# Kernel tuning notes

Hardware: AMD Instinct MI355X
Metric: run time of the kernel (lower is better)

Reference implementation:

```python
import jax, jax.numpy as jnp
import numpy as np

SCALING = 2.0      # lora_alpha / r = 32 / 16
TEMPERATURE = 1.0  # router_temperature


def setup_inputs() -> dict:
    key = jax.random.key(0)
    ks = jax.random.split(key, 7)
    B, S, D, K, R = 4, 2048, 4096, 8, 16
    # Note: torch inits lora_B to zeros; we use small random values so the
    return {
        "x": jax.random.normal(ks[0], (B, S, D), dtype=jnp.float32),
        "base_w": jax.random.normal(ks[1], (D, D), dtype=jnp.float32) * 0.02,
        "base_b": jax.random.normal(ks[2], (D,), dtype=jnp.float32) * 0.02,
        "lora_A": jax.random.normal(ks[3], (K, R, D), dtype=jnp.float32) * 0.02,
        "lora_B": jax.random.normal(ks[4], (K, D, R), dtype=jnp.float32) * 0.02,
        "router_w": jax.random.normal(ks[5], (K, D), dtype=jnp.float32) * 0.02,
        "router_b": jnp.zeros((K,), dtype=jnp.float32),
    }


def reference(x, base_w, base_b, lora_A, lora_B, router_w, router_b):
    # base_layer(x): x @ W^T + b
    base = jnp.einsum("bsd,od->bso", x, base_w) + base_b
    # router on mean-pooled sequence (x.dim()==3 branch): softmax(Linear(mean_s x))
    router_in = x.mean(axis=1)                                   # [B, D]
    logits = router_in @ router_w.T + router_b                   # [B, K]
    weights = jax.nn.softmax(logits / TEMPERATURE, axis=-1)      # [B, K]
    # grouped LoRA experts: h = A_k x, out = sum_k w_k * B_k h  (dropout p=0 -> identity)
    h = jnp.einsum("bsd,krd->bskr", x, lora_A)                   # [B, S, K, R]
    lora = jnp.einsum("bskr,kor,bk->bso", h, lora_B, weights)    # [B, S, D]
    return base + SCALING * lora
```

## Files before the change

kernel.cpp:

```cpp
#include <hip/hip_runtime.h>
#include <hip/hip_fp16.h>
#include <stdint.h>

typedef _Float16 f16;
typedef __attribute__((ext_vector_type(8))) _Float16 f16x8;
typedef __attribute__((ext_vector_type(4))) float f32x4;

#define D_DIM 4096
#define S_DIM 2048
#define M_DIM 8192
#define R_DIM 16
#define KR 128
#define KTOT 4224
#define NKT 66
#define SCALING 2.0f

#define WS_AP    0
#define WS_WP    69206016
#define WS_AH    103809024
#define WS_HP    104857600
#define WS_PART  121634816
#define WS_LG    123731968
#define WS_WS    123732096

__device__ __forceinline__ void load_lds16(const void* g, void* l) {
  __builtin_amdgcn_global_load_lds(
      (const __attribute__((address_space(1))) void*)g,
      (__attribute__((address_space(3))) void*)l, 16, 0, 0);
}

union H4 { f16 h[4]; ushort4 u; };

__global__ void conv_x(const float* __restrict__ x, f16* __restrict__ Ap,
                       float* __restrict__ part) {
  int rc = blockIdx.x;
  int cc = blockIdx.y;
  int col = cc * 1024 + threadIdx.x * 4;
  long base = (long)rc * 64 * D_DIM + col;
  float s0 = 0, s1 = 0, s2 = 0, s3 = 0;
  for (int r = 0; r < 64; ++r) {
    float4 v = *(const float4*)(x + base + (long)r * D_DIM);
    H4 t; t.h[0] = (f16)v.x; t.h[1] = (f16)v.y; t.h[2] = (f16)v.z; t.h[3] = (f16)v.w;
    *(ushort4*)((char*)Ap + ((long)(rc * 64 + r) * KTOT + col) * 2) = t.u;
    s0 += v.x; s1 += v.y; s2 += v.z; s3 += v.w;
  }
  float4 sv; sv.x = s0; sv.y = s1; sv.z = s2; sv.w = s3;
  *(float4*)(part + (long)rc * D_DIM + col) = sv;
}

__global__ void conv_w(const float* __restrict__ w, f16* __restrict__ Wp) {
  int rc = blockIdx.x;
  int cc = blockIdx.y;
  int col = cc * 1024 + threadIdx.x * 4;
  long base = (long)rc * 64 * D_DIM + col;
  for (int r = 0; r < 64; ++r) {
    float4 v = *(const float4*)(w + base + (long)r * D_DIM);
    H4 t; t.h[0] = (f16)v.x; t.h[1] = (f16)v.y; t.h[2] = (f16)v.z; t.h[3] = (f16)v.w;
    *(ushort4*)((char*)Wp + ((long)(rc * 64 + r) * KTOT + col) * 2) = t.u;
  }
}

__global__ void conv_bext(const float* __restrict__ loraB, f16* __restrict__ Wp) {
  int g = blockIdx.x * 256 + threadIdx.x;
  int n = g >> 7, kr = g & 127;
  int k = kr >> 4, r = kr & 15;
  float v = loraB[((long)k * D_DIM + n) * R_DIM + r];
  Wp[(long)n * KTOT + D_DIM + kr] = (f16)v;
}

__global__ void conv_aext(const float* __restrict__ loraA, f16* __restrict__ Ah) {
  long g = ((long)blockIdx.x * 256 + threadIdx.x) * 4;
  float4 v = *(const float4*)(loraA + g);
  H4 t; t.h[0] = (f16)v.x; t.h[1] = (f16)v.y; t.h[2] = (f16)v.z; t.h[3] = (f16)v.w;
  *(ushort4*)((char*)Ah + g * 2) = t.u;
}

__global__ void router_logits(const float* __restrict__ part, const float* __restrict__ rw,
                              const float* __restrict__ rb, float* __restrict__ logits) {
  int b = blockIdx.x >> 3, k = blockIdx.x & 7;
  const float* w = rw + k * D_DIM;
  float p = 0.f;
  for (int d = threadIdx.x; d < D_DIM; d += 256) {
    float s = 0.f;
    #pragma unroll 8
    for (int i = 0; i < 32; ++i) s += part[(long)(b * 32 + i) * D_DIM + d];
    p += s * w[d];
  }
  __shared__ float red[4];
  for (int off = 32; off; off >>= 1) p += __shfl_down(p, off);
  if ((threadIdx.x & 63) == 0) red[threadIdx.x >> 6] = p;
  __syncthreads();
  if (threadIdx.x == 0)
    logits[b * 8 + k] = (red[0] + red[1] + red[2] + red[3]) / (float)S_DIM + rb[k];
}

__global__ void router_softmax(const float* __restrict__ logits, float* __restrict__ wsc) {
  int lane = threadIdx.x;
  if (lane < 32) {
    float L = logits[lane];
    float m = L;
    m = fmaxf(m, __shfl_xor(m, 1));
    m = fmaxf(m, __shfl_xor(m, 2));
    m = fmaxf(m, __shfl_xor(m, 4));
    float e = __expf(L - m);
    float s = e;
    s += __shfl_xor(s, 1); s += __shfl_xor(s, 2); s += __shfl_xor(s, 4);
    wsc[lane] = e / s * SCALING;
  }
}

__global__ void combine_h(const float* __restrict__ hp, const float* __restrict__ wsc,
                          f16* __restrict__ Ap) {
  long g = (long)blockIdx.x * 256 + threadIdx.x;
  long row = g >> 7; int kr = (int)(g & 127);
  int b = (int)(row >> 11);
  float s = hp[g] + hp[g + 1048576] + hp[g + 2097152] + hp[g + 3145728];
  Ap[row * KTOT + D_DIM + kr] = (f16)(s * wsc[b * 8 + (kr >> 4)]);
}

__global__ __launch_bounds__(256, 2) void gemm_h(
    const f16* __restrict__ A, int lda, const f16* __restrict__ Bt, int ldb,
    int kIters, float* __restrict__ C) {
  __shared__ __align__(16) f16 As[128 * 64];
  __shared__ __align__(16) f16 Bs[128 * 64];
  int tid = threadIdx.x;
  int wave = tid >> 6, lane = tid & 63;
  long row0 = (long)blockIdx.x * 128;
  long col0 = 0;
  int wr = wave >> 1, wc = wave & 1;
  int fr = lane & 15, fq = lane >> 4;
  int srow = lane >> 3;
  int scol = (lane & 7) * 8;
  long koff = (long)blockIdx.z * 1024;

  f32x4 acc[4][4] = {};

  for (int kb = 0; kb < kIters; ++kb) {
    long kbase = (long)kb * 64 + koff;
    for (int i = 0; i < 4; ++i) {
      int seg = i * 4 + wave;
      const f16* ga = A + (row0 + seg * 8 + srow) * lda + kbase + scol;
      load_lds16(ga, (char*)As + seg * 1024);
      const f16* gb = Bt + (col0 + seg * 8 + srow) * ldb + kbase + scol;
      load_lds16(gb, (char*)Bs + seg * 1024);
    }
    __syncthreads();
    for (int ks = 0; ks < 2; ++ks) {
      int kbyte = ks * 64 + fq * 16;
      f16x8 af[4], bf[4];
      for (int mi = 0; mi < 4; ++mi)
        af[mi] = *(const f16x8*)((const char*)As + (wr * 64 + mi * 16 + fr) * 128 + kbyte);
      for (int ni = 0; ni < 4; ++ni)
        bf[ni] = *(const f16x8*)((const char*)Bs + (wc * 64 + ni * 16 + fr) * 128 + kbyte);
      for (int mi = 0; mi < 4; ++mi)
        for (int ni = 0; ni < 4; ++ni)
          acc[mi][ni] = __builtin_amdgcn_mfma_f32_16x16x32_f16(af[mi], bf[ni], acc[mi][ni], 0, 0, 0);
    }
    __syncthreads();
  }

  long zb = (long)blockIdx.z * (long)M_DIM * 128;
  for (int ni = 0; ni < 4; ++ni) {
    int col = wc * 64 + ni * 16 + fr;
    for (int mi = 0; mi < 4; ++mi) {
      long row = row0 + wr * 64 + mi * 16 + fq * 4;
      float* cp = C + zb + row * 128 + col;
      #pragma unroll
      for (int j = 0; j < 4; ++j) cp[(long)j * 128] = acc[mi][ni][j];
    }
  }
}

__device__ __forceinline__ void stage256(const f16* __restrict__ G, long row0, int ld,
                                         long kbase, char* ldsT, int tid) {
  int lr = tid >> 3;
  int sw = (((tid & 7) * 16) ^ ((lr & 7) << 4)) >> 1;
  char* wbase = ldsT + ((tid >> 6) << 10);
  #pragma unroll
  for (int j = 0; j < 4; ++j) {
    const f16* g = G + (row0 + j * 64 + lr) * (long)ld + kbase + sw;
    load_lds16(g, wbase + j * 8192);
  }
}

__global__ __launch_bounds__(512, 2) void gemm256(
    const f16* __restrict__ A, int lda, const f16* __restrict__ Bt, int ldb,
    int nkt, const float* __restrict__ bias, float* __restrict__ C, int ldc) {
  __shared__ __align__(16) char smem[131072];
  int tid = threadIdx.x;
  int wave = tid >> 6, lane = tid & 63;
  int wr = wave >> 2, wc = wave & 3;
  int fr = lane & 15, fq = lane >> 4;

  int flat = blockIdx.x;
  int wg = (flat & 7) * 64 + (flat >> 3);
  long row0 = (long)(wg >> 4) * 256;
  long col0 = (long)(wg & 15) * 256;

  f32x4 acc[8][4] = {};

  stage256(A,  row0, lda, 0,  smem,          tid);
  stage256(Bt, col0, ldb, 0,  smem + 32768,  tid);
  stage256(A,  row0, lda, 64, smem + 65536,  tid);
  stage256(Bt, col0, ldb, 64, smem + 98304,  tid);
  asm volatile("s_waitcnt vmcnt(8)" ::: "memory");
  asm volatile("s_barrier" ::: "memory");

  int cur = 0;
  int sw = (fr & 7) << 4;
  for (int t = 0; t < nkt; ++t) {
    const char* Ab = smem + cur * 65536;
    const char* Bb = Ab + 32768;
    #pragma unroll
    for (int qm = 0; qm < 2; ++qm) {
      f16x8 af[4][2];
      #pragma unroll
      for (int m2 = 0; m2 < 4; ++m2) {
        int row = wr * 128 + (qm * 4 + m2) * 16 + fr;
        af[m2][0] = *(const f16x8*)(Ab + row * 128 + ((fq * 16) ^ sw));
        af[m2][1] = *(const f16x8*)(Ab + row * 128 + ((64 + fq * 16) ^ sw));
      }
      #pragma unroll
      for (int qn = 0; qn < 2; ++qn) {
        f16x8 bf[2][2];
        #pragma unroll
        for (int n2 = 0; n2 < 2; ++n2) {
          int rowb = wc * 64 + (qn * 2 + n2) * 16 + fr;
          bf[n2][0] = *(const f16x8*)(Bb + rowb * 128 + ((fq * 16) ^ sw));
          bf[n2][1] = *(const f16x8*)(Bb + rowb * 128 + ((64 + fq * 16) ^ sw));
        }
        #pragma unroll
        for (int m2 = 0; m2 < 4; ++m2)
          #pragma unroll
          for (int n2 = 0; n2 < 2; ++n2) {
            f32x4* a = &acc[qm * 4 + m2][qn * 2 + n2];
            *a = __builtin_amdgcn_mfma_f32_16x16x32_f16(af[m2][0], bf[n2][0], *a, 0, 0, 0);
            *a = __builtin_amdgcn_mfma_f32_16x16x32_f16(af[m2][1], bf[n2][1], *a, 0, 0, 0);
          }
      }
    }
    asm volatile("s_barrier" ::: "memory");
    if (t + 2 < nkt) {
      stage256(A,  row0, lda, (long)(t + 2) * 64, smem + cur * 65536,         tid);
      stage256(Bt, col0, ldb, (long)(t + 2) * 64, smem + cur * 65536 + 32768, tid);
      asm volatile("s_waitcnt vmcnt(8)" ::: "memory");
    } else {
      asm volatile("s_waitcnt vmcnt(0)" ::: "memory");
    }
    asm volatile("s_barrier" ::: "memory");
    cur ^= 1;
  }

  #pragma unroll
  for (int ni = 0; ni < 4; ++ni) {
    long col = col0 + wc * 64 + ni * 16 + fr;
    float bv = bias[col];
    #pragma unroll
    for (int mi = 0; mi < 8; ++mi) {
      long row = row0 + wr * 128 + mi * 16 + fq * 4;
      float* cp = C + row * ldc + col;
      #pragma unroll
      for (int j = 0; j < 4; ++j) cp[(long)j * ldc] = acc[mi][ni][j] + bv;
    }
  }
}

extern "C" void kernel_launch(void* const* d_in, const int* in_sizes, int n_in,
                              void* d_out, int out_size, void* d_ws, size_t ws_size,
                              hipStream_t stream) {
  (void)in_sizes; (void)n_in; (void)out_size; (void)ws_size;
  const float* x        = (const float*)d_in[0];
  const float* base_w   = (const float*)d_in[1];
  const float* base_b   = (const float*)d_in[2];
  const float* lora_A   = (const float*)d_in[3];
  const float* lora_B   = (const float*)d_in[4];
  const float* router_w = (const float*)d_in[5];
  const float* router_b = (const float*)d_in[6];
  float* out = (float*)d_out;

  char* ws = (char*)d_ws;
  f16* Ap       = (f16*)(ws + WS_AP);
  f16* Wp       = (f16*)(ws + WS_WP);
  f16* Ah       = (f16*)(ws + WS_AH);
  float* hp     = (float*)(ws + WS_HP);
  float* part   = (float*)(ws + WS_PART);
  float* logits = (float*)(ws + WS_LG);
  float* wsc    = (float*)(ws + WS_WS);

  conv_x<<<dim3(128, 4), 256, 0, stream>>>(x, Ap, part);
  conv_w<<<dim3(64, 4), 256, 0, stream>>>(base_w, Wp);
  conv_bext<<<2048, 256, 0, stream>>>(lora_B, Wp);
  conv_aext<<<512, 256, 0, stream>>>(lora_A, Ah);
  router_logits<<<32, 256, 0, stream>>>(part, router_w, router_b, logits);
  router_softmax<<<1, 64, 0, stream>>>(logits, wsc);
  gemm_h<<<dim3(64, 1, 4), 256, 0, stream>>>(Ap, KTOT, Ah, D_DIM, 16, hp);
  combine_h<<<4096, 256, 0, stream>>>(hp, wsc, Ap);
  gemm256<<<512, 512, 0, stream>>>(Ap, KTOT, Wp, KTOT, NKT, base_b, out, D_DIM);
}
```

Baseline: 589.0 us.

## Double-buffer and swizzle LDS in LoRA-A GEMM; raise wave priority during MFMA

Replaces the simple single-buffered gemm_h with gemm_h2. The new kernel uses two LDS stages with async global-to-LDS prefetch two tiles ahead and an XOR swizzle on LDS addresses to avoid bank conflicts, so global loads can overlap MFMA work. It also adds s_setprio around the MFMA sections in both gemm_h2 and the main gemm256 to favour compute waves. The cost is more LDS per block (64KB), which may limit occupancy.

New measurement: 588.7 us. About the same (-0.1%).

```diff
diff --git a/kernel.cpp b/kernel.cpp
--- a/kernel.cpp
+++ b/kernel.cpp
@@ -118,59 +118,6 @@
   Ap[row * KTOT + D_DIM + kr] = (f16)(s * wsc[b * 8 + (kr >> 4)]);
 }
 
-__global__ __launch_bounds__(256, 2) void gemm_h(
-    const f16* __restrict__ A, int lda, const f16* __restrict__ Bt, int ldb,
-    int kIters, float* __restrict__ C) {
-  __shared__ __align__(16) f16 As[128 * 64];
-  __shared__ __align__(16) f16 Bs[128 * 64];
-  int tid = threadIdx.x;
-  int wave = tid >> 6, lane = tid & 63;
-  long row0 = (long)blockIdx.x * 128;
-  long col0 = 0;
-  int wr = wave >> 1, wc = wave & 1;
-  int fr = lane & 15, fq = lane >> 4;
-  int srow = lane >> 3;
-  int scol = (lane & 7) * 8;
-  long koff = (long)blockIdx.z * 1024;
-
-  f32x4 acc[4][4] = {};
-
-  for (int kb = 0; kb < kIters; ++kb) {
-    long kbase = (long)kb * 64 + koff;
-    for (int i = 0; i < 4; ++i) {
-      int seg = i * 4 + wave;
-      const f16* ga = A + (row0 + seg * 8 + srow) * lda + kbase + scol;
-      load_lds16(ga, (char*)As + seg * 1024);
-      const f16* gb = Bt + (col0 + seg * 8 + srow) * ldb + kbase + scol;
-      load_lds16(gb, (char*)Bs + seg * 1024);
-    }
-    __syncthreads();
-    for (int ks = 0; ks < 2; ++ks) {
-      int kbyte = ks * 64 + fq * 16;
-      f16x8 af[4], bf[4];
-      for (int mi = 0; mi < 4; ++mi)
-        af[mi] = *(const f16x8*)((const char*)As + (wr * 64 + mi * 16 + fr) * 128 + kbyte);
-      for (int ni = 0; ni < 4; ++ni)
-        bf[ni] = *(const f16x8*)((const char*)Bs + (wc * 64 + ni * 16 + fr) * 128 + kbyte);
-      for (int mi = 0; mi < 4; ++mi)
-        for (int ni = 0; ni < 4; ++ni)
-          acc[mi][ni] = __builtin_amdgcn_mfma_f32_16x16x32_f16(af[mi], bf[ni], acc[mi][ni], 0, 0, 0);
-    }
-    __syncthreads();
-  }
-
-  long zb = (long)blockIdx.z * (long)M_DIM * 128;
-  for (int ni = 0; ni < 4; ++ni) {
-    int col = wc * 64 + ni * 16 + fr;
-    for (int mi = 0; mi < 4; ++mi) {
-      long row = row0 + wr * 64 + mi * 16 + fq * 4;
-      float* cp = C + zb + row * 128 + col;
-      #pragma unroll
-      for (int j = 0; j < 4; ++j) cp[(long)j * 128] = acc[mi][ni][j];
-    }
-  }
-}
-
 __device__ __forceinline__ void stage256(const f16* __restrict__ G, long row0, int ld,
                                          long kbase, char* ldsT, int tid) {
   int lr = tid >> 3;
@@ -182,6 +129,86 @@
     load_lds16(g, wbase + j * 8192);
   }
 }
+__device__ __forceinline__ void stage128(const f16* __restrict__ G, long row0, int ld,
+                                         long kbase, char* ldsT, int tid) {
+  int lr = tid >> 3;
+  int sw = (((tid & 7) * 16) ^ ((lr & 7) << 4)) >> 1;
+  char* wbase = ldsT + ((tid >> 6) << 10);
+  #pragma unroll
+  for (int j = 0; j < 4; ++j) {
+    const f16* g = G + (row0 + j * 32 + lr) * (long)ld + kbase + sw;
+    load_lds16(g, wbase + j * 4096);
+  }
+}
+
+__global__ __launch_bounds__(256, 2) void gemm_h2(
+    const f16* __restrict__ A, int lda, const f16* __restrict__ Bt, int ldb,
+    float* __restrict__ hp) {
+  __shared__ __align__(16) char smem[65536];
+  int tid = threadIdx.x;
+  int wave = tid >> 6, lane = tid & 63;
+  int wr = wave >> 1, wc = wave & 1;
+  int fr = lane & 15, fq = lane >> 4;
+  long row0 = (long)blockIdx.x * 128;
+  long koff = (long)blockIdx.y * 1024;
+
+  f32x4 acc[4][4] = {};
+
+  stage128(A,  row0, lda, koff,      smem,         tid);
+  stage128(Bt, 0,    ldb, koff,      smem + 16384, tid);
+  stage128(A,  row0, lda, koff + 64, smem + 32768, tid);
+  stage128(Bt, 0,    ldb, koff + 64, smem + 49152, tid);
+  asm volatile("s_waitcnt vmcnt(8)" ::: "memory");
+  asm volatile("s_barrier" ::: "memory");
+
+  int cur = 0;
+  int sw = (fr & 7) << 4;
+  for (int t = 0; t < 16; ++t) {
+    const char* Ab = smem + cur * 32768;
+    const char* Bb = Ab + 16384;
+    __builtin_amdgcn_s_setprio(1);
+    #pragma unroll
+    for (int ks = 0; ks < 2; ++ks) {
+      int kb = ks * 64 + fq * 16;
+      f16x8 af[4], bf[4];
+      #pragma unroll
+      for (int mi = 0; mi < 4; ++mi)
+        af[mi] = *(const f16x8*)(Ab + (wr * 64 + mi * 16 + fr) * 128 + (kb ^ sw));
+      #pragma unroll
+      for (int ni = 0; ni < 4; ++ni)
+        bf[ni] = *(const f16x8*)(Bb + (wc * 64 + ni * 16 + fr) * 128 + (kb ^ sw));
+      #pragma unroll
+      for (int mi = 0; mi < 4; ++mi)
+        #pragma unroll
+        for (int ni = 0; ni < 4; ++ni)
+          acc[mi][ni] = __builtin_amdgcn_mfma_f32_16x16x32_f16(af[mi], bf[ni], acc[mi][ni], 0, 0, 0);
+    }
+    __builtin_amdgcn_s_setprio(0);
+    asm volatile("s_barrier" ::: "memory");
+    if (t + 2 < 16) {
+      stage128(A,  row0, lda, koff + (t + 2) * 64, smem + cur * 32768,         tid);
+      stage128(Bt, 0,    ldb, koff + (t + 2) * 64, smem + cur * 32768 + 16384, tid);
+      asm volatile("s_waitcnt vmcnt(8)" ::: "memory");
+    } else {
+      asm volatile("s_waitcnt vmcnt(0)" ::: "memory");
+    }
+    asm volatile("s_barrier" ::: "memory");
+    cur ^= 1;
+  }
+
+  long zb = (long)blockIdx.y * (long)M_DIM * 128;
+  #pragma unroll
+  for (int ni = 0; ni < 4; ++ni) {
+    int col = wc * 64 + ni * 16 + fr;
+    #pragma unroll
+    for (int mi = 0; mi < 4; ++mi) {
+      long row = row0 + wr * 64 + mi * 16 + fq * 4;
+      float* cp = hp + zb + row * 128 + col;
+      #pragma unroll
+      for (int j = 0; j < 4; ++j) cp[(long)j * 128] = acc[mi][ni][j];
+    }
+  }
+}
 
 __global__ __launch_bounds__(512, 2) void gemm256(
     const f16* __restrict__ A, int lda, const f16* __restrict__ Bt, int ldb,
@@ -211,6 +238,7 @@
   for (int t = 0; t < nkt; ++t) {
     const char* Ab = smem + cur * 65536;
     const char* Bb = Ab + 32768;
+    __builtin_amdgcn_s_setprio(1);
     #pragma unroll
     for (int qm = 0; qm < 2; ++qm) {
       f16x8 af[4][2];
@@ -239,6 +267,7 @@
           }
       }
     }
+    __builtin_amdgcn_s_setprio(0);
     asm volatile("s_barrier" ::: "memory");
     if (t + 2 < nkt) {
       stage256(A,  row0, lda, (long)(t + 2) * 64, smem + cur * 65536,         tid);
@@ -293,7 +322,7 @@
   conv_aext<<<512, 256, 0, stream>>>(lora_A, Ah);
   router_logits<<<32, 256, 0, stream>>>(part, router_w, router_b, logits);
   router_softmax<<<1, 64, 0, stream>>>(logits, wsc);
-  gemm_h<<<dim3(64, 1, 4), 256, 0, stream>>>(Ap, KTOT, Ah, D_DIM, 16, hp);
+  gemm_h2<<<dim3(64, 4), 256, 0, stream>>>(Ap, KTOT, Ah, D_DIM, hp);
   combine_h<<<4096, 256, 0, stream>>>(hp, wsc, Ap);
   gemm256<<<512, 512, 0, stream>>>(Ap, KTOT, Wp, KTOT, NKT, base_b, out, D_DIM);
 }
```
